# Optimization experiments

Measured on AMD Instinct MI355X. Metric: run time of the kernel, lower is better.

Reference implementation:

```python
import jax, jax.numpy as jnp
import numpy as np

NUM_HEADS = 16

def _rmsnorm(x, w):
    eps = jnp.finfo(x.dtype).eps  # torch nn.RMSNorm default eps
    ms = jnp.mean(x * x, axis=-1, keepdims=True)
    return x * jax.lax.rsqrt(ms + eps) * w

def _heads(x):
    B, S, D = x.shape
    return x.reshape(B, S, NUM_HEADS, D // NUM_HEADS)

def _attn(q, k, v):
    # q:[B,Sq,H,D] k,v:[B,Sk,H,D]; non-causal softmax attention
    scale = 1.0 / np.sqrt(q.shape[-1]).astype(np.float32)
    s = jnp.einsum('bqhd,bkhd->bhqk', q, k) * scale
    p = jax.nn.softmax(s, axis=-1)
    return jnp.einsum('bhqk,bkhd->bqhd', p, v)

def _gate(ctx, W1, b1, W2, b2):
    # Linear -> SiLU -> Linear(dim->1) -> sigmoid ; returns [B,S,1]
    h = jax.nn.silu(ctx @ W1.T + b1)
    return jax.nn.sigmoid(h @ W2.T + b2)

def setup_inputs() -> dict:
    key = jax.random.key(0)
    ks = jax.random.split(key, 20)
    B, Sq, Sk, St, dim = 4, 512, 2048, 512, 1024
    n = lambda k, shp, s=1.0: jax.random.normal(k, shp, jnp.float32) * s
    W = lambda k, o, i: n(k, (o, i), 0.02)
    return {
        'queries': n(ks[0], (B, Sq, dim)),
        'context_visual': n(ks[1], (B, Sk, dim)),
        'context_text': n(ks[2], (B, St, dim)),
        'w_norm_q': jnp.ones((dim,), jnp.float32),
        'w_norm_v': jnp.ones((dim,), jnp.float32),
        'w_norm_t': jnp.ones((dim,), jnp.float32),
        'Wq': W(ks[3], dim, dim), 'bq': n(ks[4], (dim,), 0.02),
        'Wk_vis': W(ks[5], dim, dim), 'bk_vis': jnp.zeros((dim,), jnp.float32),
        'Wv_vis': W(ks[6], dim, dim), 'bv_vis': jnp.zeros((dim,), jnp.float32),
        'Wk_text': W(ks[7], dim, dim), 'bk_text': jnp.zeros((dim,), jnp.float32),
        'Wv_text': W(ks[8], dim, dim), 'bv_text': jnp.zeros((dim,), jnp.float32),
        'Wg1v': W(ks[9], dim, dim), 'bg1v': jnp.zeros((dim,), jnp.float32),
        'Wg2v': W(ks[10], 1, dim), 'bg2v': jnp.zeros((1,), jnp.float32),
        'Wg1t': W(ks[11], dim, dim), 'bg1t': jnp.zeros((dim,), jnp.float32),
        'Wg2t': W(ks[12], 1, dim), 'bg2t': jnp.zeros((1,), jnp.float32),
        'Wo': W(ks[13], dim, dim), 'bo': jnp.zeros((dim,), jnp.float32),
    }

def reference(queries, context_visual, context_text,
              w_norm_q, w_norm_v, w_norm_t,
              Wq, bq, Wk_vis, bk_vis, Wv_vis, bv_vis,
              Wk_text, bk_text, Wv_text, bv_text,
              Wg1v, bg1v, Wg2v, bg2v, Wg1t, bg1t, Wg2t, bg2t,
              Wo, bo):
    residual = queries
    qn = _rmsnorm(queries, w_norm_q)
    cv = _rmsnorm(context_visual, w_norm_v)
    ct = _rmsnorm(context_text, w_norm_t)
    q = _heads(qn @ Wq.T + bq)
    k_vis = _heads(cv @ Wk_vis.T + bk_vis)
    v_vis = _heads(cv @ Wv_vis.T + bv_vis)
    v_vis = v_vis * _gate(cv, Wg1v, bg1v, Wg2v, bg2v)[..., None]  # [B,Sk,1,1]
    h = _attn(q, k_vis, v_vis)
    k_text = _heads(ct @ Wk_text.T + bk_text)
    v_text = _heads(ct @ Wv_text.T + bv_text)
    v_text = v_text * _gate(ct, Wg1t, bg1t, Wg2t, bg2t)[..., None]
    h = h + _attn(q, k_text, v_text)
    B, Sq, H, D = h.shape
    out = h.reshape(B, Sq, H * D) @ Wo.T + bo  # dropout p=0 -> identity
    return residual + out
```

## Files before the change

kernel.cpp:

```cpp
#include <hip/hip_runtime.h>
#include <hip/hip_bf16.h>

typedef __attribute__((ext_vector_type(4))) float f32x4;
typedef __attribute__((ext_vector_type(8))) short s16x8;
typedef __attribute__((ext_vector_type(4))) short s16x4;
using bf16 = __hip_bfloat16;

static constexpr int BB  = 4;
static constexpr int SQ  = 512;
static constexpr int SKV = 2048;
static constexpr int SKT = 512;
static constexpr int DIM = 1024;
static constexpr int NH  = 16;
static constexpr int HD  = 64;

#define MFMA32(A,B,C) __builtin_amdgcn_mfma_f32_16x16x32_bf16(A,B,C,0,0,0)

#if __has_builtin(__builtin_amdgcn_mfma_f32_16x16x16_bf16)
  #define MFMA16(A,B,C) __builtin_amdgcn_mfma_f32_16x16x16_bf16(A,B,C,0,0,0)
  #define HAVE_X16 1
#elif __has_builtin(__builtin_amdgcn_mfma_f32_16x16x16bf16_1k)
  #define MFMA16(A,B,C) __builtin_amdgcn_mfma_f32_16x16x16bf16_1k(A,B,C,0,0,0)
  #define HAVE_X16 1
#else
  #define HAVE_X16 0
#endif

#define SBAR() asm volatile("s_barrier" ::: "memory")

__device__ __forceinline__ float b2f(short s) {
  unsigned int u = ((unsigned int)(unsigned short)s) << 16;
  float f; __builtin_memcpy(&f, &u, 4); return f;
}
__device__ __forceinline__ short f2s(float f) {
  bf16 h = __float2bfloat16(f); short s; __builtin_memcpy(&s, &h, 2); return s;
}

__device__ __forceinline__ void gload16(const void* g, void* l) {
  __builtin_amdgcn_global_load_lds(
      (const __attribute__((address_space(1))) void*)g,
      (__attribute__((address_space(3))) void*)l, 16, 0, 0);
}

static constexpr float QSCALE = 0.180336880111120426f;

struct PrepArgs {
  const float* csrc[10]; bf16* cdst[10]; int cn[10];
  const float* nx[3]; const float* nw[3]; bf16* ny[3];
};
__global__ __launch_bounds__(256) void prep_kernel(PrepArgs a) {
  const int bx = blockIdx.x;
  if (bx < 10240) {
    const int y = bx >> 10;
    const int i = ((bx & 1023) * 256 + threadIdx.x) * 4;
    if (i >= a.cn[y]) return;
    const float4 v = *(const float4*)(a.csrc[y] + i);
    bf16* d = a.cdst[y] + i;
    d[0] = __float2bfloat16(v.x); d[1] = __float2bfloat16(v.y);
    d[2] = __float2bfloat16(v.z); d[3] = __float2bfloat16(v.w);
    return;
  }
  const int j = bx - 10240;
  int t, row;
  if (j < 2048) { t = 0; row = j; }
  else if (j < 10240) { t = 1; row = j - 2048; }
  else { t = 2; row = j - 10240; }
  const float* x = a.nx[t] + (size_t)row * DIM;
  const float4 v = *(const float4*)(x + threadIdx.x * 4);
  float ss = v.x*v.x + v.y*v.y + v.z*v.z + v.w*v.w;
  #pragma unroll
  for (int m = 32; m >= 1; m >>= 1) ss += __shfl_xor(ss, m);
  __shared__ float red[4];
  if ((threadIdx.x & 63) == 0) red[threadIdx.x >> 6] = ss;
  __syncthreads();
  ss = red[0] + red[1] + red[2] + red[3];
  const float sc = rsqrtf(ss * (1.0f / DIM) + 1.1920928955078125e-07f);
  const float4 w = *(const float4*)(a.nw[t] + threadIdx.x * 4);
  bf16* y = a.ny[t] + (size_t)row * DIM + threadIdx.x * 4;
  y[0] = __float2bfloat16(v.x * sc * w.x);
  y[1] = __float2bfloat16(v.y * sc * w.y);
  y[2] = __float2bfloat16(v.z * sc * w.z);
  y[3] = __float2bfloat16(v.w * sc * w.w);
}

struct PSlot { const bf16* A; const bf16* W; const float* bias;
               bf16* Cb; int epi; int sksh; };
struct PArgs { PSlot s[7]; };

__global__ __launch_bounds__(512, 2) void proj256(PArgs a) {
  __shared__ char lds[131072];
  const int tid = threadIdx.x, lane = tid & 63, wave = tid >> 6;
  const int m16 = lane & 15, g16 = lane >> 4;
  const int wm = wave >> 2, wn = wave & 3;

  const int i = (blockIdx.x & 7) * 64 + (blockIdx.x >> 3);
  int slot, rem;
  if (i < 384) { slot = i >> 7; rem = i & 127; }
  else { const int j = i - 384; slot = 3 + (j >> 5); rem = j & 31; }
  const PSlot S = a.s[slot];
  const int bn = rem & 3, bm = rem >> 2;

  const bf16* Ab = S.A + (size_t)bm * 256 * DIM;
  const bf16* Wb = S.W + (size_t)bn * 256 * DIM;

  auto stageA = [&](int k0, int buf) {
    #pragma unroll
    for (int q = 0; q < 4; ++q) {
      const int idx = q * 512 + tid;
      const int row = idx >> 3, g = (idx & 7) ^ (row & 7);
      gload16(Ab + (size_t)row * DIM + k0 + g * 8,
              &lds[buf * 65536 + q * 8192 + wave * 1024]);
    }
  };
  auto stageB = [&](int k0, int buf) {
    #pragma unroll
    for (int q = 0; q < 4; ++q) {
      const int idx = q * 512 + tid;
      const int row = idx >> 3, g = (idx & 7) ^ (row & 7);
      gload16(Wb + (size_t)row * DIM + k0 + g * 8,
              &lds[buf * 65536 + 32768 + q * 8192 + wave * 1024]);
    }
  };

  f32x4 acc[8][4];
  #pragma unroll
  for (int x = 0; x < 8; ++x)
    #pragma unroll
    for (int y = 0; y < 4; ++y)
      #pragma unroll
      for (int r = 0; r < 4; ++r) acc[x][y][r] = 0.0f;

  stageA(0, 0); stageB(0, 0);
  stageA(64, 1); stageB(64, 1);
  asm volatile("s_waitcnt vmcnt(8)" ::: "memory");
  SBAR();

  constexpr int NT = DIM / 64;
  for (int t = 0; t < NT; ++t) {
    const int buf = t & 1;
    const char* A0 = &lds[buf * 65536];
    const char* B0 = A0 + 32768;
    s16x8 af[4][2], bf0[2][2], bf1[2][2];

    #pragma unroll
    for (int mi = 0; mi < 4; ++mi) {
      const int row = wm * 128 + mi * 16 + m16;
      #pragma unroll
      for (int ks = 0; ks < 2; ++ks)
        af[mi][ks] = *(const s16x8*)(A0 + row * 128 + (((ks*4+g16) ^ (m16 & 7)) * 16));
    }
    #pragma unroll
    for (int ni = 0; ni < 2; ++ni) {
      const int row = wn * 64 + ni * 16 + m16;
      #pragma unroll
      for (int ks = 0; ks < 2; ++ks)
        bf0[ni][ks] = *(const s16x8*)(B0 + row * 128 + (((ks*4+g16) ^ (m16 & 7)) * 16));
    }
    SBAR();
    __builtin_amdgcn_s_setprio(1);
    #pragma unroll
    for (int mi = 0; mi < 4; ++mi)
      #pragma unroll
      for (int ni = 0; ni < 2; ++ni) {
        acc[mi][ni] = MFMA32(af[mi][0], bf0[ni][0], acc[mi][ni]);
        acc[mi][ni] = MFMA32(af[mi][1], bf0[ni][1], acc[mi][ni]);
      }
    __builtin_amdgcn_s_setprio(0);
    SBAR();

    #pragma unroll
    for (int ni = 0; ni < 2; ++ni) {
      const int row = wn * 64 + 32 + ni * 16 + m16;
      #pragma unroll
      for (int ks = 0; ks < 2; ++ks)
        bf1[ni][ks] = *(const s16x8*)(B0 + row * 128 + (((ks*4+g16) ^ (m16 & 7)) * 16));
    }
    SBAR();
    __builtin_amdgcn_s_setprio(1);
    #pragma unroll
    for (int mi = 0; mi < 4; ++mi)
      #pragma unroll
      for (int ni = 0; ni < 2; ++ni) {
        acc[mi][2+ni] = MFMA32(af[mi][0], bf1[ni][0], acc[mi][2+ni]);
        acc[mi][2+ni] = MFMA32(af[mi][1], bf1[ni][1], acc[mi][2+ni]);
      }
    __builtin_amdgcn_s_setprio(0);
    SBAR();

    if (t + 2 < NT) stageB((t + 2) * 64, buf);
    #pragma unroll
    for (int mi = 0; mi < 4; ++mi) {
      const int row = wm * 128 + 64 + mi * 16 + m16;
      #pragma unroll
      for (int ks = 0; ks < 2; ++ks)
        af[mi][ks] = *(const s16x8*)(A0 + row * 128 + (((ks*4+g16) ^ (m16 & 7)) * 16));
    }
    SBAR();
    __builtin_amdgcn_s_setprio(1);
    #pragma unroll
    for (int mi = 0; mi < 4; ++mi)
      #pragma unroll
      for (int ni = 0; ni < 2; ++ni) {
        acc[4+mi][ni] = MFMA32(af[mi][0], bf0[ni][0], acc[4+mi][ni]);
        acc[4+mi][ni] = MFMA32(af[mi][1], bf0[ni][1], acc[4+mi][ni]);
      }
    __builtin_amdgcn_s_setprio(0);
    SBAR();

    if (t + 2 < NT) stageA((t + 2) * 64, buf);
    __builtin_amdgcn_s_setprio(1);
    #pragma unroll
    for (int mi = 0; mi < 4; ++mi)
      #pragma unroll
      for (int ni = 0; ni < 2; ++ni) {
        acc[4+mi][2+ni] = MFMA32(af[mi][0], bf1[ni][0], acc[4+mi][2+ni]);
        acc[4+mi][2+ni] = MFMA32(af[mi][1], bf1[ni][1], acc[4+mi][2+ni]);
      }
    __builtin_amdgcn_s_setprio(0);
    if (t < NT - 2)       { asm volatile("s_waitcnt vmcnt(8)" ::: "memory"); }
    else if (t == NT - 2) { asm volatile("s_waitcnt vmcnt(0)" ::: "memory"); }
    SBAR();
  }

  const int r0 = bm * 256 + wm * 128, c0 = bn * 256 + wn * 64;
  if (S.epi >= 3) {
    const float sc = (S.epi == 3) ? QSCALE : 1.0f;
    const int msk = (1 << S.sksh) - 1;
    #pragma unroll
    for (int ng = 0; ng < 4; ++ng) {
      const int col = c0 + ng * 16 + m16;
      const int hh = col >> 6, d = col & 63;
      const float bv = S.bias[col];
      #pragma unroll
      for (int mg = 0; mg < 8; ++mg) {
        const int rowb = r0 + mg * 16 + g16 * 4;
        #pragma unroll
        for (int r = 0; r < 4; ++r) {
          const int m = rowb + r;
          const int bb2 = m >> S.sksh, tok = m & msk;
          S.Cb[(((size_t)(bb2 * NH + hh) << S.sksh) + tok) * HD + d] =
              __float2bfloat16((acc[mg][ng][r] + bv) * sc);
        }
      }
    }
  } else {
    #pragma unroll
    for (int ng = 0; ng < 4; ++ng) {
      const int col = c0 + ng * 16 + m16;
      const float bv = S.bias[col];
      #pragma unroll
      for (int mg = 0; mg < 8; ++mg) {
        const int rowb = r0 + mg * 16 + g16 * 4;
        #pragma unroll
        for (int r = 0; r < 4; ++r) {
          float v = acc[mg][ng][r] + bv;
          const size_t idx = (size_t)(rowb + r) * DIM + col;
          if (S.epi == 1) { v = v / (1.0f + __expf(-v)); S.Cb[idx] = __float2bfloat16(v); }
          else            { S.Cb[idx] = __float2bfloat16(v); }
        }
      }
    }
  }
}

struct GSlot { const bf16* A; const bf16* W; const float* bias;
               const float* resid; float* Cf; };
__global__ __launch_bounds__(256) void gemm_out(GSlot S) {
  constexpr int K = DIM;
  __shared__ alignas(16) char sA[4096];
  __shared__ alignas(16) char sB[8192];
  const int tid = threadIdx.x, lane = tid & 63, wave = tid >> 6;
  const int bm = blockIdx.x, bn = blockIdx.y;
  const int m16 = lane & 15, g16 = lane >> 4;

  f32x4 acc[4][2];
  #pragma unroll
  for (int i = 0; i < 4; ++i)
    #pragma unroll
    for (int j = 0; j < 2; ++j)
      #pragma unroll
      for (int r = 0; r < 4; ++r) acc[i][j][r] = 0.0f;

  const bf16* Ab = S.A + (size_t)bm * 64 * K;
  const bf16* Wb = S.W + (size_t)bn * 128 * K;

  for (int t = 0; t < K / 32; ++t) {
    const int k0 = t * 32;
    {
      const int row = tid >> 2, sg = (tid & 3) ^ (row & 3);
      gload16(Ab + (size_t)row * K + k0 + sg * 8, &sA[wave * 1024]);
    }
    #pragma unroll
    for (int p = 0; p < 2; ++p) {
      const int idx = p * 256 + tid;
      const int row = idx >> 2, sg = (idx & 3) ^ (row & 3);
      gload16(Wb + (size_t)row * K + k0 + sg * 8, &sB[p * 4096 + wave * 1024]);
    }
    __syncthreads();
    s16x8 af[4], bfr[2];
    #pragma unroll
    for (int mi = 0; mi < 4; ++mi) {
      const int row = mi * 16 + m16;
      af[mi] = *(const s16x8*)(&sA[row * 64 + (g16 ^ (m16 & 3)) * 16]);
    }
    #pragma unroll
    for (int ni = 0; ni < 2; ++ni) {
      const int row = wave * 32 + ni * 16 + m16;
      bfr[ni] = *(const s16x8*)(&sB[row * 64 + (g16 ^ (m16 & 3)) * 16]);
    }
    #pragma unroll
    for (int mi = 0; mi < 4; ++mi)
      #pragma unroll
      for (int ni = 0; ni < 2; ++ni)
        acc[mi][ni] = MFMA32(af[mi], bfr[ni], acc[mi][ni]);
    __syncthreads();
  }

  const int r0 = bm * 64, c0 = bn * 128 + wave * 32;
  #pragma unroll
  for (int ni = 0; ni < 2; ++ni) {
    const int col = c0 + ni * 16 + m16;
    const float bv = S.bias[col];
    #pragma unroll
    for (int mi = 0; mi < 4; ++mi) {
      const int rowb = r0 + mi * 16 + g16 * 4;
      #pragma unroll
      for (int r = 0; r < 4; ++r) {
        const size_t idx = (size_t)(rowb + r) * DIM + col;
        S.Cf[idx] = acc[mi][ni][r] + bv + S.resid[idx];
      }
    }
  }
}

__global__ __launch_bounds__(256) void gate2_kernel(
    const bf16* __restrict__ g1v, const bf16* __restrict__ w2v,
    const float* __restrict__ b2v, float* __restrict__ gv,
    const bf16* __restrict__ g1t, const bf16* __restrict__ w2t,
    const float* __restrict__ b2t, float* __restrict__ gt)
{
  const int lane = threadIdx.x & 63, wave = threadIdx.x >> 6;
  int row = blockIdx.x * 4 + wave;
  const bf16* x; const bf16* w2; const float* b2; float* gate;
  if (row < BB * SKV) { x = g1v + (size_t)row * DIM; w2 = w2v; b2 = b2v; gate = gv + row; }
  else { row -= BB * SKV; x = g1t + (size_t)row * DIM; w2 = w2t; b2 = b2t; gate = gt + row; }
  float sum = 0.0f;
  #pragma unroll
  for (int c = 0; c < 2; ++c) {
    const int i0 = c * 512 + lane * 8;
    const s16x8 xv = *(const s16x8*)(x + i0);
    const s16x8 wv = *(const s16x8*)(w2 + i0);
    #pragma unroll
    for (int j = 0; j < 8; ++j) sum += b2f(xv[j]) * b2f(wv[j]);
  }
  #pragma unroll
  for (int m = 32; m >= 1; m >>= 1) sum += __shfl_xor(sum, m);
  if (lane == 0) *gate = 1.0f / (1.0f + __expf(-(sum + b2[0])));
}

__global__ __launch_bounds__(256) void vtrans2_kernel(
    const bf16* __restrict__ Vv, const float* __restrict__ gv, bf16* __restrict__ VTv,
    const bf16* __restrict__ Vt, const float* __restrict__ gt, bf16* __restrict__ VTt)
{
  __shared__ alignas(16) short tile[64][72];
  int kt = blockIdx.x;
  const bf16* V; const float* gate; bf16* VT; int Sk;
  if (kt < SKV / 64) { V = Vv; gate = gv; VT = VTv; Sk = SKV; }
  else { kt -= SKV / 64; V = Vt; gate = gt; VT = VTt; Sk = SKT; }
  const int h = blockIdx.y, b = blockIdx.z;
  const int tid = threadIdx.x;
  #pragma unroll
  for (int i = 0; i < 2; ++i) {
    const int c = tid + i * 256;
    const int kr = c >> 3, d0 = (c & 7) * 8;
    const float g = gate[(size_t)b * Sk + kt * 64 + kr];
    const s16x8 v = *(const s16x8*)(V + ((size_t)(b*Sk + kt*64 + kr)*NH + h)*HD + d0);
    #pragma unroll
    for (int j = 0; j < 8; ++j) tile[kr][d0 + j] = f2s(b2f(v[j]) * g);
  }
  __syncthreads();
  #pragma unroll
  for (int i = 0; i < 2; ++i) {
    const int c = tid + i * 256;
    const int d = c >> 3, k0 = (c & 7) * 8;
    s16x8 v;
    #pragma unroll
    for (int j = 0; j < 8; ++j) v[j] = tile[k0 + j][d];
    *(s16x8*)(VT + ((size_t)(b*NH + h)*HD + d)*Sk + kt*64 + k0) = v;
  }
}

__global__ __launch_bounds__(256, 4) void attn_kernel(
    const bf16* __restrict__ Qh,
    const bf16* __restrict__ K1h, const bf16* __restrict__ VT1,
    const bf16* __restrict__ K2h, const bf16* __restrict__ VT2,
    bf16* __restrict__ Hout)
{
  __shared__ alignas(16) char sK[2][8192];
  __shared__ alignas(16) char sVT[2][8192];
  const int tid = threadIdx.x, lane = tid & 63, wave = tid >> 6;
  const int hb = blockIdx.x;
  const int h = hb & 15, b = hb >> 4;
  const int wq = wave & 1, hf = wave >> 1;
  const int q0 = blockIdx.y * 32 + wq * 16;
  const int m16 = lane & 15, g16 = lane >> 4;

  const bf16* qrow = Qh + ((size_t)(b*NH + h)*SQ + q0 + m16)*HD;
  const s16x8 qf0 = *(const s16x8*)(qrow + g16 * 8);
  const s16x8 qf1 = *(const s16x8*)(qrow + 32 + g16 * 8);

  const bf16* K1b  = K1h + (size_t)(b*NH + h) * SKV * HD;
  const bf16* K2b  = K2h + (size_t)(b*NH + h) * SKT * HD;
  const bf16* VT1b = VT1 + (size_t)(b*NH + h) * HD * SKV;
  const bf16* VT2b = VT2 + (size_t)(b*NH + h) * HD * SKT;

  auto stage = [&](const bf16* Kb, const bf16* VTb, int Sk, int b0, int b1) {
    #pragma unroll
    for (int p = 0; p < 2; ++p) {
      const int idx = p * 256 + tid;
      const int r = idx >> 3, g = (idx & 7) ^ (r & 7);
      gload16(Kb  + (size_t)(b0 + r) * HD + g * 8, &sK[0][p * 4096 + wave * 1024]);
      gload16(Kb  + (size_t)(b1 + r) * HD + g * 8, &sK[1][p * 4096 + wave * 1024]);
      gload16(VTb + (size_t)r * Sk + b0 + g * 8,   &sVT[0][p * 4096 + wave * 1024]);
      gload16(VTb + (size_t)r * Sk + b1 + g * 8,   &sVT[1][p * 4096 + wave * 1024]);
    }
  };

  float of[4][4];
  #pragma unroll
  for (int i = 0; i < 4; ++i)
    #pragma unroll
    for (int r = 0; r < 4; ++r) of[i][r] = 0.0f;

  f32x4 o[4];
  float mx, l;
  auto reset_state = [&]() {
    #pragma unroll
    for (int i = 0; i < 4; ++i)
      #pragma unroll
      for (int r = 0; r < 4; ++r) o[i][r] = 0.0f;
    mx = -1e30f; l = 0.0f;
  };

  auto chunk = [&]() {
    const char* kbase = &sK[hf][0];
    const char* vbase = &sVT[hf][0];
    f32x4 s[4];
    #pragma unroll
    for (int nt = 0; nt < 4; ++nt) {
      const char* kr = kbase + (nt * 16 + m16) * 128;
      const s16x8 kf0 = *(const s16x8*)(kr + ((g16    ) ^ (m16 & 7)) * 16);
      const s16x8 kf1 = *(const s16x8*)(kr + ((4 + g16) ^ (m16 & 7)) * 16);
      f32x4 a2; a2[0] = 0; a2[1] = 0; a2[2] = 0; a2[3] = 0;
      a2 = MFMA32(kf0, qf0, a2);
      a2 = MFMA32(kf1, qf1, a2);
      s[nt] = a2;
    }
    float mc = s[0][0];
    #pragma unroll
    for (int nt = 0; nt < 4; ++nt)
      #pragma unroll
      for (int r = 0; r < 4; ++r) mc = fmaxf(mc, s[nt][r]);
    mc = fmaxf(mc, __shfl_xor(mc, 16));
    mc = fmaxf(mc, __shfl_xor(mc, 32));
    const float mnew = fmaxf(mx, mc);
    const float alpha = exp2f(mx - mnew);
    mx = mnew;
    float p[4][4]; float rs = 0.0f;
    #pragma unroll
    for (int nt = 0; nt < 4; ++nt)
      #pragma unroll
      for (int r = 0; r < 4; ++r) { p[nt][r] = exp2f(s[nt][r] - mnew); rs += p[nt][r]; }
    rs += __shfl_xor(rs, 16);
    rs += __shfl_xor(rs, 32);
    l = l * alpha + rs;
    float av[4];
    #pragma unroll
    for (int r = 0; r < 4; ++r) av[r] = __shfl(alpha, g16 * 4 + r);
    #pragma unroll
    for (int nd = 0; nd < 4; ++nd)
      #pragma unroll
      for (int r = 0; r < 4; ++r) o[nd][r] *= av[r];
#if HAVE_X16
    #pragma unroll
    for (int nt = 0; nt < 4; ++nt) {
      s16x4 pa;
      pa[0] = f2s(p[nt][0]); pa[1] = f2s(p[nt][1]);
      pa[2] = f2s(p[nt][2]); pa[3] = f2s(p[nt][3]);
      #pragma unroll
      for (int nd = 0; nd < 4; ++nd) {
        const int d = nd * 16 + m16;
        const int g = (nt * 2 + (g16 >> 1)) ^ (m16 & 7);
        const s16x4 vf = *(const s16x4*)(vbase + d * 128 + g * 16 + (g16 & 1) * 8);
        o[nd] = MFMA16(pa, vf, o[nd]);
      }
    }
#endif
  };

  auto merge_flush = [&]() {
    __syncthreads();
    float* mo = (float*)&sK[0][0];
    float* ml = (float*)&sVT[0][0];
    if (hf) {
      #pragma unroll
      for (int nd = 0; nd < 4; ++nd)
        #pragma unroll
        for (int r = 0; r < 4; ++r)
          mo[(wq * 16 + g16 * 4 + r) * 64 + nd * 16 + m16] = o[nd][r];
      if (g16 == 0) { ml[(wq * 2 + 0) * 16 + m16] = mx; ml[(wq * 2 + 1) * 16 + m16] = l; }
    }
    __syncthreads();
    if (!hf) {
      const float mb = ml[(wq * 2 + 0) * 16 + m16];
      const float lb = ml[(wq * 2 + 1) * 16 + m16];
      const float ms = fmaxf(mx, mb);
      const float aA = exp2f(mx - ms), aB = exp2f(mb - ms);
      const float lt = l * aA + lb * aB;
      float aAv[4], aBv[4], ltv[4];
      #pragma unroll
      for (int r = 0; r < 4; ++r) {
        aAv[r] = __shfl(aA, g16 * 4 + r);
        aBv[r] = __shfl(aB, g16 * 4 + r);
        ltv[r] = __shfl(lt, g16 * 4 + r);
      }
      #pragma unroll
      for (int nd = 0; nd < 4; ++nd)
        #pragma unroll
        for (int r = 0; r < 4; ++r) {
          const float ob = mo[(wq * 16 + g16 * 4 + r) * 64 + nd * 16 + m16];
          of[nd][r] += (o[nd][r] * aAv[r] + ob * aBv[r]) / ltv[r];
        }
    }
    __syncthreads();
  };

  reset_state();
  for (int c = 0; c < SKV / 128; ++c) {
    stage(K1b, VT1b, SKV, c * 64, 1024 + c * 64);
    __syncthreads();
    chunk();
    __syncthreads();
  }
  merge_flush();

  reset_state();
  for (int c = 0; c < SKT / 128; ++c) {
    stage(K2b, VT2b, SKT, c * 64, 256 + c * 64);
    __syncthreads();
    chunk();
    __syncthreads();
  }
  merge_flush();

  if (!hf) {
    #pragma unroll
    for (int nd = 0; nd < 4; ++nd)
      #pragma unroll
      for (int r = 0; r < 4; ++r) {
        const int row = q0 + g16 * 4 + r;
        Hout[((size_t)(b*SQ + row)*NH + h)*HD + nd*16 + m16] =
            __float2bfloat16(of[nd][r]);
      }
  }
}

extern "C" void kernel_launch(void* const* d_in, const int* in_sizes, int n_in,
                              void* d_out, int out_size, void* d_ws, size_t ws_size,
                              hipStream_t stream)
{
  const float* queries = (const float*)d_in[0];
  const float* ctx_v   = (const float*)d_in[1];
  const float* ctx_t   = (const float*)d_in[2];
  const float* w_nq = (const float*)d_in[3];
  const float* w_nv = (const float*)d_in[4];
  const float* w_nt = (const float*)d_in[5];
  const float* Wq   = (const float*)d_in[6];  const float* bq   = (const float*)d_in[7];
  const float* Wk_v = (const float*)d_in[8];  const float* bk_v = (const float*)d_in[9];
  const float* Wv_v = (const float*)d_in[10]; const float* bv_v = (const float*)d_in[11];
  const float* Wk_t = (const float*)d_in[12]; const float* bk_t = (const float*)d_in[13];
  const float* Wv_t = (const float*)d_in[14]; const float* bv_t = (const float*)d_in[15];
  const float* Wg1v = (const float*)d_in[16]; const float* bg1v = (const float*)d_in[17];
  const float* Wg2v = (const float*)d_in[18]; const float* bg2v = (const float*)d_in[19];
  const float* Wg1t = (const float*)d_in[20]; const float* bg1t = (const float*)d_in[21];
  const float* Wg2t = (const float*)d_in[22]; const float* bg2t = (const float*)d_in[23];
  const float* Wo   = (const float*)d_in[24]; const float* bo   = (const float*)d_in[25];

  char* ws = (char*)d_ws;
  size_t off = 0;
  auto alloc = [&](size_t n) { void* p = ws + off; off += (n + 255) & ~(size_t)255; return p; };

  const size_t MATB = (size_t)DIM * DIM * 2;
  bf16* WqB   = (bf16*)alloc(MATB);
  bf16* WkvB  = (bf16*)alloc(MATB);
  bf16* WvvB  = (bf16*)alloc(MATB);
  bf16* WktB  = (bf16*)alloc(MATB);
  bf16* WvtB  = (bf16*)alloc(MATB);
  bf16* Wg1vB = (bf16*)alloc(MATB);
  bf16* Wg1tB = (bf16*)alloc(MATB);
  bf16* WoB   = (bf16*)alloc(MATB);
  bf16* Wg2vB = (bf16*)alloc(2048);
  bf16* Wg2tB = (bf16*)alloc(2048);

  bf16* qn  = (bf16*)alloc((size_t)BB*SQ*DIM*2);
  bf16* cv  = (bf16*)alloc((size_t)BB*SKV*DIM*2);
  bf16* ct  = (bf16*)alloc((size_t)BB*SKT*DIM*2);
  bf16* qb  = (bf16*)alloc((size_t)BB*SQ*DIM*2);
  bf16* kvB = (bf16*)alloc((size_t)BB*SKV*DIM*2);
  bf16* ktB = (bf16*)alloc((size_t)BB*SKT*DIM*2);
  bf16* vtV = (bf16*)alloc((size_t)BB*SKV*DIM*2);
  bf16* vtT = (bf16*)alloc((size_t)BB*SKT*DIM*2);
  bf16* vScrV = (bf16*)alloc((size_t)BB*SKV*DIM*2);
  bf16* vScrT = (bf16*)alloc((size_t)BB*SKT*DIM*2);
  bf16* g1V   = (bf16*)alloc((size_t)BB*SKV*DIM*2);
  bf16* g1T   = (bf16*)alloc((size_t)BB*SKT*DIM*2);
  float* gateV = (float*)alloc((size_t)BB*SKV*4);
  float* gateT = (float*)alloc((size_t)BB*SKT*4);
  bf16* hB  = (bf16*)alloc((size_t)BB*SQ*DIM*2);
  (void)ws_size; (void)n_in; (void)in_sizes; (void)out_size;

  PrepArgs pr;
  const float* wsrc[10] = {Wq, Wk_v, Wv_v, Wk_t, Wv_t, Wg1v, Wg1t, Wo, Wg2v, Wg2t};
  bf16* wdst[10] = {WqB, WkvB, WvvB, WktB, WvtB, Wg1vB, Wg1tB, WoB, Wg2vB, Wg2tB};
  for (int i = 0; i < 10; ++i) {
    pr.csrc[i] = wsrc[i]; pr.cdst[i] = wdst[i];
    pr.cn[i] = (i < 8) ? DIM * DIM : DIM;
  }
  pr.nx[0] = queries; pr.nx[1] = ctx_v; pr.nx[2] = ctx_t;
  pr.nw[0] = w_nq;    pr.nw[1] = w_nv;  pr.nw[2] = w_nt;
  pr.ny[0] = qn;      pr.ny[1] = cv;    pr.ny[2] = ct;
  prep_kernel<<<dim3(10240 + 12288), 256, 0, stream>>>(pr);

  PArgs pa;
  pa.s[0] = {cv, WkvB,  bk_v, kvB,   4, 11};
  pa.s[1] = {cv, WvvB,  bv_v, vScrV, 0, 0};
  pa.s[2] = {cv, Wg1vB, bg1v, g1V,   1, 0};
  pa.s[3] = {qn, WqB,   bq,   qb,    3, 9};
  pa.s[4] = {ct, WktB,  bk_t, ktB,   4, 9};
  pa.s[5] = {ct, WvtB,  bv_t, vScrT, 0, 0};
  pa.s[6] = {ct, Wg1tB, bg1t, g1T,   1, 0};
  proj256<<<dim3(512), 512, 0, stream>>>(pa);

  gate2_kernel<<<dim3((BB*SKV + BB*SKT) / 4), 256, 0, stream>>>(
      g1V, Wg2vB, bg2v, gateV, g1T, Wg2tB, bg2t, gateT);
  vtrans2_kernel<<<dim3(SKV/64 + SKT/64, NH, BB), 256, 0, stream>>>(
      vScrV, gateV, vtV, vScrT, gateT, vtT);

  attn_kernel<<<dim3(NH*BB, SQ/32), 256, 0, stream>>>(qb, kvB, vtV, ktB, vtT, hB);

  GSlot go{hB, WoB, bo, queries, (float*)d_out};
  gemm_out<<<dim3(BB*SQ/64, 8), 256, 0, stream>>>(go);
}
```

Baseline: 203.4 us.

## Double-buffer attention K/V loads, widen blocks, and coalesce projection epilogue via LDS

```diff
diff --git a/kernel.cpp b/kernel.cpp
--- a/kernel.cpp
+++ b/kernel.cpp
@@ -18,12 +18,10 @@
 
 #if __has_builtin(__builtin_amdgcn_mfma_f32_16x16x16_bf16)
   #define MFMA16(A,B,C) __builtin_amdgcn_mfma_f32_16x16x16_bf16(A,B,C,0,0,0)
-  #define HAVE_X16 1
 #elif __has_builtin(__builtin_amdgcn_mfma_f32_16x16x16bf16_1k)
   #define MFMA16(A,B,C) __builtin_amdgcn_mfma_f32_16x16x16bf16_1k(A,B,C,0,0,0)
-  #define HAVE_X16 1
 #else
-  #define HAVE_X16 0
+  #define MFMA16(A,B,C) (C)
 #endif
 
 #define SBAR() asm volatile("s_barrier" ::: "memory")
@@ -222,42 +220,46 @@
     SBAR();
   }
 
-  const int r0 = bm * 256 + wm * 128, c0 = bn * 256 + wn * 64;
-  if (S.epi >= 3) {
-    const float sc = (S.epi == 3) ? QSCALE : 1.0f;
-    const int msk = (1 << S.sksh) - 1;
-    #pragma unroll
-    for (int ng = 0; ng < 4; ++ng) {
-      const int col = c0 + ng * 16 + m16;
-      const int hh = col >> 6, d = col & 63;
-      const float bv = S.bias[col];
-      #pragma unroll
-      for (int mg = 0; mg < 8; ++mg) {
-        const int rowb = r0 + mg * 16 + g16 * 4;
-        #pragma unroll
-        for (int r = 0; r < 4; ++r) {
-          const int m = rowb + r;
-          const int bb2 = m >> S.sksh, tok = m & msk;
-          S.Cb[(((size_t)(bb2 * NH + hh) << S.sksh) + tok) * HD + d] =
-              __float2bfloat16((acc[mg][ng][r] + bv) * sc);
-        }
-      }
-    }
-  } else {
-    #pragma unroll
-    for (int ng = 0; ng < 4; ++ng) {
-      const int col = c0 + ng * 16 + m16;
-      const float bv = S.bias[col];
-      #pragma unroll
-      for (int mg = 0; mg < 8; ++mg) {
-        const int rowb = r0 + mg * 16 + g16 * 4;
-        #pragma unroll
-        for (int r = 0; r < 4; ++r) {
-          float v = acc[mg][ng][r] + bv;
-          const size_t idx = (size_t)(rowb + r) * DIM + col;
-          if (S.epi == 1) { v = v / (1.0f + __expf(-v)); S.Cb[idx] = __float2bfloat16(v); }
-          else            { S.Cb[idx] = __float2bfloat16(v); }
-        }
+  #pragma unroll
+  for (int ng = 0; ng < 4; ++ng) {
+    const int col_l = wn * 64 + ng * 16 + m16;
+    const float bv = S.bias[bn * 256 + col_l];
+    #pragma unroll
+    for (int mg = 0; mg < 8; ++mg) {
+      #pragma unroll
+      for (int r = 0; r < 4; ++r) {
+        const int row_l = wm * 128 + mg * 16 + g16 * 4 + r;
+        float v = acc[mg][ng][r] + bv;
+        if (S.epi == 1)      v = v / (1.0f + __expf(-v));
+        else if (S.epi == 3) v = v * QSCALE;
+        const int byte = row_l * 512 + ((col_l * 2) ^ (((row_l >> 2) & 7) << 4));
+        *(short*)(&lds[byte]) = f2s(v);
+      }
+    }
+  }
+  __syncthreads();
+  {
+    const int row_l = tid >> 1, half = tid & 1;
+    const int m = bm * 256 + row_l;
+    const int xr = ((row_l >> 2) & 7) << 4;
+    if (S.epi >= 3) {
+      const int msk = (1 << S.sksh) - 1;
+      const int bb2 = m >> S.sksh, tok = m & msk;
+      #pragma unroll
+      for (int j = 0; j < 16; ++j) {
+        const int colbyte = half * 256 + j * 16;
+        const s16x8 val = *(const s16x8*)(&lds[row_l * 512 + (colbyte ^ xr)]);
+        const int col_g = bn * 256 + half * 128 + j * 8;
+        const int hh = col_g >> 6, d = col_g & 63;
+        *(s16x8*)(&S.Cb[(((size_t)(bb2 * NH + hh) << S.sksh) + tok) * HD + d]) = val;
+      }
+    } else {
+      #pragma unroll
+      for (int j = 0; j < 16; ++j) {
+        const int colbyte = half * 256 + j * 16;
+        const s16x8 val = *(const s16x8*)(&lds[row_l * 512 + (colbyte ^ xr)]);
+        const int col_g = bn * 256 + half * 128 + j * 8;
+        *(s16x8*)(&S.Cb[(size_t)m * DIM + col_g]) = val;
       }
     }
   }
@@ -390,19 +392,19 @@
   }
 }
 
-__global__ __launch_bounds__(256, 4) void attn_kernel(
+__global__ __launch_bounds__(512, 2) void attn_kernel(
     const bf16* __restrict__ Qh,
     const bf16* __restrict__ K1h, const bf16* __restrict__ VT1,
     const bf16* __restrict__ K2h, const bf16* __restrict__ VT2,
     bf16* __restrict__ Hout)
 {
-  __shared__ alignas(16) char sK[2][8192];
-  __shared__ alignas(16) char sVT[2][8192];
+  __shared__ alignas(16) char sK[2][2][8192];
+  __shared__ alignas(16) char sVT[2][2][8192];
   const int tid = threadIdx.x, lane = tid & 63, wave = tid >> 6;
   const int hb = blockIdx.x;
   const int h = hb & 15, b = hb >> 4;
-  const int wq = wave & 1, hf = wave >> 1;
-  const int q0 = blockIdx.y * 32 + wq * 16;
+  const int wq = wave & 3, hf = wave >> 2;
+  const int q0 = blockIdx.y * 64 + wq * 16;
   const int m16 = lane & 15, g16 = lane >> 4;
 
   const bf16* qrow = Qh + ((size_t)(b*NH + h)*SQ + q0 + m16)*HD;
@@ -414,37 +416,33 @@
   const bf16* VT1b = VT1 + (size_t)(b*NH + h) * HD * SKV;
   const bf16* VT2b = VT2 + (size_t)(b*NH + h) * HD * SKT;
 
-  auto stage = [&](const bf16* Kb, const bf16* VTb, int Sk, int b0, int b1) {
-    #pragma unroll
-    for (int p = 0; p < 2; ++p) {
-      const int idx = p * 256 + tid;
-      const int r = idx >> 3, g = (idx & 7) ^ (r & 7);
-      gload16(Kb  + (size_t)(b0 + r) * HD + g * 8, &sK[0][p * 4096 + wave * 1024]);
-      gload16(Kb  + (size_t)(b1 + r) * HD + g * 8, &sK[1][p * 4096 + wave * 1024]);
-      gload16(VTb + (size_t)r * Sk + b0 + g * 8,   &sVT[0][p * 4096 + wave * 1024]);
-      gload16(VTb + (size_t)r * Sk + b1 + g * 8,   &sVT[1][p * 4096 + wave * 1024]);
-    }
+  constexpr int NC1 = SKV / 128, NC = NC1 + SKT / 128;
+
+  auto stage = [&](int c, int buf) {
+    const int ctx = (c >= NC1);
+    const bf16* Kb  = ctx ? K2b  : K1b;
+    const bf16* VTb = ctx ? VT2b : VT1b;
+    const int Sk = ctx ? SKT : SKV;
+    const int cc = ctx ? c - NC1 : c;
+    const int b0 = cc * 64, b1 = (Sk >> 1) + cc * 64;
+    const int r = tid >> 3, g = (tid & 7) ^ (r & 7);
+    gload16(Kb  + (size_t)(b0 + r) * HD + g * 8, &sK[buf][0][wave * 1024]);
+    gload16(Kb  + (size_t)(b1 + r) * HD + g * 8, &sK[buf][1][wave * 1024]);
+    gload16(VTb + (size_t)r * Sk + b0 + g * 8,   &sVT[buf][0][wave * 1024]);
+    gload16(VTb + (size_t)r * Sk + b1 + g * 8,   &sVT[buf][1][wave * 1024]);
   };
 
-  float of[4][4];
+  f32x4 o[4], ov[4];
+  float mx, l, mxv, lv;
   #pragma unroll
   for (int i = 0; i < 4; ++i)
     #pragma unroll
-    for (int r = 0; r < 4; ++r) of[i][r] = 0.0f;
-
-  f32x4 o[4];
-  float mx, l;
-  auto reset_state = [&]() {
-    #pragma unroll
-    for (int i = 0; i < 4; ++i)
-      #pragma unroll
-      for (int r = 0; r < 4; ++r) o[i][r] = 0.0f;
-    mx = -1e30f; l = 0.0f;
-  };
-
-  auto chunk = [&]() {
-    const char* kbase = &sK[hf][0];
-    const char* vbase = &sVT[hf][0];
+    for (int r = 0; r < 4; ++r) { o[i][r] = 0.0f; ov[i][r] = 0.0f; }
+  mx = -1e30f; l = 0.0f; mxv = -1e30f; lv = 0.0f;
+
+  auto chunk = [&](int buf) {
+    const char* kbase = &sK[buf][hf][0];
+    const char* vbase = &sVT[buf][hf][0];
     f32x4 s[4];
     #pragma unroll
     for (int nt = 0; nt < 4; ++nt) {
@@ -481,7 +479,6 @@
     for (int nd = 0; nd < 4; ++nd)
       #pragma unroll
       for (int r = 0; r < 4; ++r) o[nd][r] *= av[r];
-#if HAVE_X16
     #pragma unroll
     for (int nt = 0; nt < 4; ++nt) {
       s16x4 pa;
@@ -495,28 +492,59 @@
         o[nd] = MFMA16(pa, vf, o[nd]);
       }
     }
-#endif
   };
 
-  auto merge_flush = [&]() {
-    __syncthreads();
-    float* mo = (float*)&sK[0][0];
-    float* ml = (float*)&sVT[0][0];
-    if (hf) {
+  stage(0, 0);
+  asm volatile("s_waitcnt vmcnt(0)" ::: "memory");
+  SBAR();
+
+  int buf = 0;
+  for (int c = 0; c < NC; ++c) {
+    if (c + 1 < NC) stage(c + 1, buf ^ 1);
+    chunk(buf);
+    if (c == NC1 - 1) {
+      #pragma unroll
+      for (int nd = 0; nd < 4; ++nd) ov[nd] = o[nd];
+      mxv = mx; lv = l;
       #pragma unroll
       for (int nd = 0; nd < 4; ++nd)
         #pragma unroll
-        for (int r = 0; r < 4; ++r)
-          mo[(wq * 16 + g16 * 4 + r) * 64 + nd * 16 + m16] = o[nd][r];
-      if (g16 == 0) { ml[(wq * 2 + 0) * 16 + m16] = mx; ml[(wq * 2 + 1) * 16 + m16] = l; }
-    }
-    __syncthreads();
-    if (!hf) {
-      const float mb = ml[(wq * 2 + 0) * 16 + m16];
-      const float lb = ml[(wq * 2 + 1) * 16 + m16];
-      const float ms = fmaxf(mx, mb);
-      const float aA = exp2f(mx - ms), aB = exp2f(mb - ms);
-      const float lt = l * aA + lb * aB;
+        for (int r = 0; r < 4; ++r) o[nd][r] = 0.0f;
+      mx = -1e30f; l = 0.0f;
+    }
+    asm volatile("s_waitcnt vmcnt(0)" ::: "memory");
+    SBAR();
+    buf ^= 1;
+  }
+
+  float* mo = (float*)&sK[0][0][0];
+  float* ml = (float*)&sVT[0][0][0];
+  if (hf) {
+    #pragma unroll
+    for (int nd = 0; nd < 4; ++nd)
+      #pragma unroll
+      for (int r = 0; r < 4; ++r) {
+        const int rl = wq * 16 + g16 * 4 + r;
+        mo[rl * 64 + nd * 16 + m16]        = ov[nd][r];
+        mo[4096 + rl * 64 + nd * 16 + m16] = o[nd][r];
+      }
+    if (g16 == 0) {
+      ml[(wq * 4 + 0) * 16 + m16] = mxv; ml[(wq * 4 + 1) * 16 + m16] = lv;
+      ml[(wq * 4 + 2) * 16 + m16] = mx;  ml[(wq * 4 + 3) * 16 + m16] = l;
+    }
+  }
+  __syncthreads();
+  if (!hf) {
+    float of[4][4];
+    #pragma unroll
+    for (int ctx = 0; ctx < 2; ++ctx) {
+      const float mb = ml[(wq * 4 + ctx * 2 + 0) * 16 + m16];
+      const float lb = ml[(wq * 4 + ctx * 2 + 1) * 16 + m16];
+      const float ma = ctx ? mx : mxv;
+      const float la = ctx ? l  : lv;
+      const float ms = fmaxf(ma, mb);
+      const float aA = exp2f(ma - ms), aB = exp2f(mb - ms);
+      const float lt = la * aA + lb * aB;
       float aAv[4], aBv[4], ltv[4];
       #pragma unroll
       for (int r = 0; r < 4; ++r) {
@@ -528,32 +556,13 @@
       for (int nd = 0; nd < 4; ++nd)
         #pragma unroll
         for (int r = 0; r < 4; ++r) {
-          const float ob = mo[(wq * 16 + g16 * 4 + r) * 64 + nd * 16 + m16];
-          of[nd][r] += (o[nd][r] * aAv[r] + ob * aBv[r]) / ltv[r];
+          const int rl = wq * 16 + g16 * 4 + r;
+          const float ob = mo[ctx * 4096 + rl * 64 + nd * 16 + m16];
+          const float oa = ctx ? o[nd][r] : ov[nd][r];
+          const float res = (oa * aAv[r] + ob * aBv[r]) / ltv[r];
+          if (ctx == 0) of[nd][r] = res; else of[nd][r] += res;
         }
     }
-    __syncthreads();
-  };
-
-  reset_state();
-  for (int c = 0; c < SKV / 128; ++c) {
-    stage(K1b, VT1b, SKV, c * 64, 1024 + c * 64);
-    __syncthreads();
-    chunk();
-    __syncthreads();
-  }
-  merge_flush();
-
-  reset_state();
-  for (int c = 0; c < SKT / 128; ++c) {
-    stage(K2b, VT2b, SKT, c * 64, 256 + c * 64);
-    __syncthreads();
-    chunk();
-    __syncthreads();
-  }
-  merge_flush();
-
-  if (!hf) {
     #pragma unroll
     for (int nd = 0; nd < 4; ++nd)
       #pragma unroll
@@ -646,7 +655,7 @@
   vtrans2_kernel<<<dim3(SKV/64 + SKT/64, NH, BB), 256, 0, stream>>>(
       vScrV, gateV, vtV, vScrT, gateT, vtT);
 
-  attn_kernel<<<dim3(NH*BB, SQ/32), 256, 0, stream>>>(qb, kvB, vtV, ktB, vtT, hB);
+  attn_kernel<<<dim3(NH*BB, SQ/64), 512, 0, stream>>>(qb, kvB, vtV, ktB, vtT, hB);
 
   GSlot go{hB, WoB, bo, queries, (float*)d_out};
   gemm_out<<<dim3(BB*SQ/64, 8), 256, 0, stream>>>(go);
```

New measurement: 217.2 us. +6.8%, slower.
